# Optimization experiments

Hardware: AMD Instinct MI355X
Metric: run time of the kernel (lower is better)

The kernel has to match this reference:

```python
import jax, jax.numpy as jnp
import numpy as np

D_MODEL, H, G = 2048, 32, 8
D_K = D_MODEL // H          # 64
GROUP_SIZE = H // G         # 4
B, S = 2, 2048


def setup_inputs() -> dict:
    key = jax.random.key(0)
    ks = jax.random.split(key, 9)
    sd = 1.0 / np.sqrt(D_MODEL)
    x = jax.random.normal(ks[0], (B, S, D_MODEL), dtype=jnp.float32)
    Wq = jax.random.normal(ks[1], (D_MODEL, D_MODEL), dtype=jnp.float32) * sd
    bq = jax.random.normal(ks[2], (D_MODEL,), dtype=jnp.float32) * 0.01
    Wk = jax.random.normal(ks[3], (D_MODEL, G * D_K), dtype=jnp.float32) * sd
    bk = jax.random.normal(ks[4], (G * D_K,), dtype=jnp.float32) * 0.01
    Wv = jax.random.normal(ks[5], (D_MODEL, G * D_K), dtype=jnp.float32) * sd
    bv = jax.random.normal(ks[6], (G * D_K,), dtype=jnp.float32) * 0.01
    Wo = jax.random.normal(ks[7], (D_MODEL, D_MODEL), dtype=jnp.float32) * sd
    bo = jax.random.normal(ks[8], (D_MODEL,), dtype=jnp.float32) * 0.01
    return {"x": x, "Wq": Wq, "bq": bq, "Wk": Wk, "bk": bk,
            "Wv": Wv, "bv": bv, "Wo": Wo, "bo": bo}


def reference(x, Wq, bq, Wk, bk, Wv, bv, Wo, bo):
    Bsz, Sln, _ = x.shape
    # projections
    Q = (x @ Wq + bq).reshape(Bsz, Sln, H, D_K).transpose(0, 2, 1, 3)   # [B,h,S,dk]
    K = (x @ Wk + bk).reshape(Bsz, Sln, G, D_K).transpose(0, 2, 1, 3)   # [B,g,S,dk]
    V = (x @ Wv + bv).reshape(Bsz, Sln, G, D_K).transpose(0, 2, 1, 3)   # [B,g,S,dk]
    # reshape Q into groups: [B, g, group_size, S, dk]; K/V broadcast over group dim
    Qg = Q.reshape(Bsz, G, GROUP_SIZE, Sln, D_K)
    scores = jnp.einsum('bgmqd,bgkd->bgmqk', Qg, K) / jnp.sqrt(jnp.float32(D_K))
    attn = jax.nn.softmax(scores, axis=-1)                              # [B,g,gs,S,S]
    out = jnp.einsum('bgmqk,bgkd->bgmqd', attn, V)                      # [B,g,gs,S,dk]
    out = out.reshape(Bsz, H, Sln, D_K).transpose(0, 2, 1, 3).reshape(Bsz, Sln, D_MODEL)
    return out @ Wo + bo
```

## Files before the change

### kernel.cpp

```cpp
#include <hip/hip_runtime.h>
#include <stdint.h>

#define DMODEL 2048
#define NHEADS 32
#define NGRP 8
#define DKH 64
#define BATCH 2
#define SEQ 2048
#define MTOT (BATCH*SEQ)

typedef unsigned short u16;
typedef __bf16 bf16x8 __attribute__((ext_vector_type(8)));
typedef float f32x4 __attribute__((ext_vector_type(4)));
typedef _Float16 f16x4 __attribute__((ext_vector_type(4)));
typedef _Float16 f16x8 __attribute__((ext_vector_type(8)));

#define QSCALE 0.18033688011112042f

__device__ __forceinline__ u16 f2bf(float f){
    uint32_t x = __float_as_uint(f);
    x += 0x7FFFu + ((x >> 16) & 1u);
    return (u16)(x >> 16);
}

__device__ __forceinline__ void gld_lds16(const u16* g, u16* l){
    __builtin_amdgcn_global_load_lds(
        (const __attribute__((address_space(1))) uint32_t*)g,
        (__attribute__((address_space(3))) uint32_t*)l, 16, 0, 0);
}

__global__ void cvt_fused(const float* __restrict__ x, u16* __restrict__ xb,
                          const float* __restrict__ Wq, const float* __restrict__ Wk,
                          const float* __restrict__ Wv, const float* __restrict__ Wo,
                          u16* __restrict__ WqT, u16* __restrict__ WkT,
                          u16* __restrict__ WvT, u16* __restrict__ WoT){
    __shared__ float t[32][33];
    int bid = blockIdx.x;
    if (bid < 8192){
        int i = (bid * 256 + threadIdx.x) * 4;
        float4 v = *(const float4*)(x + i);
        uint32_t lo = (uint32_t)f2bf(v.x) | ((uint32_t)f2bf(v.y) << 16);
        uint32_t hi = (uint32_t)f2bf(v.z) | ((uint32_t)f2bf(v.w) << 16);
        *(uint2*)(xb + i) = make_uint2(lo, hi);
        return;
    }
    int id = bid - 8192;
    int bx = id % 160, ky = id / 160;
    const float* W; u16* T; int N; int cx;
    if (bx < 64)      { W = Wq; T = WqT; N = 2048; cx = bx; }
    else if (bx < 80) { W = Wk; T = WkT; N = 512;  cx = bx - 64; }
    else if (bx < 96) { W = Wv; T = WvT; N = 512;  cx = bx - 80; }
    else              { W = Wo; T = WoT; N = 2048; cx = bx - 96; }
    int tx = threadIdx.x & 31, ty = threadIdx.x >> 5;
    int n0 = cx * 32, k0 = ky * 32;
#pragma unroll
    for (int i = 0; i < 4; i++)
        t[ty*4+i][tx] = W[(size_t)(k0 + ty*4 + i) * N + n0 + tx];
    __syncthreads();
#pragma unroll
    for (int i = 0; i < 4; i++)
        T[(size_t)(n0 + ty*4 + i) * DMODEL + k0 + tx] = f2bf(t[tx][ty*4+i]);
}

template<int EPI, int MINW>
__global__ __launch_bounds__(256, MINW) void gemm_nt(
    const u16* __restrict__ A, const u16* __restrict__ Bt,
    const float* __restrict__ bias0, const float* __restrict__ bias1, const float* __restrict__ bias2,
    void* __restrict__ out0, void* __restrict__ out1, void* __restrict__ out2, int Kn)
{
    __shared__ alignas(16) u16 As[128*32];
    __shared__ alignas(16) u16 Bs[128*32];
    const int tid  = threadIdx.x;
    const int w    = tid >> 6, lane = tid & 63, quad = lane >> 4, l16 = lane & 15;
    const int wr   = w >> 1,  wc   = w & 1;

    int bid = blockIdx.y * gridDim.x + blockIdx.x;
    int nwg = gridDim.x * gridDim.y;
    int cpx = nwg >> 3;
    int sbid = (bid & 7) * cpx + (bid >> 3);
    int bx = sbid % gridDim.x, by = sbid / gridDim.x;
    const int m0 = bx * 128, n0 = by * 128;

    const int arow = lane >> 2, acol = (lane & 3) * 8;

    const u16* ga = A  + (size_t)(m0 + w*32 + arow) * Kn + acol;
    const u16* gb = Bt + (size_t)(n0 + w*32 + arow) * Kn + acol;
    u16* la = As + (w*32) * 32;
    u16* lb = Bs + (w*32) * 32;

    f32x4 acc[4][4] = {};

    for (int k0 = 0; k0 < Kn; k0 += 32){
        __syncthreads();
        gld_lds16(ga + k0,                  la);
        gld_lds16(ga + k0 + (size_t)16*Kn,  la + 16*32);
        gld_lds16(gb + k0,                  lb);
        gld_lds16(gb + k0 + (size_t)16*Kn,  lb + 16*32);
        __syncthreads();
        bf16x8 af[4], bfr[4];
#pragma unroll
        for (int t = 0; t < 4; t++)
            af[t]  = *(const bf16x8*)(As + (wr*64 + t*16 + l16)*32 + quad*8);
#pragma unroll
        for (int t = 0; t < 4; t++)
            bfr[t] = *(const bf16x8*)(Bs + (wc*64 + t*16 + l16)*32 + quad*8);
#pragma unroll
        for (int tm = 0; tm < 4; tm++)
#pragma unroll
            for (int tn = 0; tn < 4; tn++)
                acc[tm][tn] = __builtin_amdgcn_mfma_f32_16x16x32_bf16(af[tm], bfr[tn], acc[tm][tn], 0, 0, 0);
    }

#pragma unroll
    for (int tn = 0; tn < 4; tn++){
        int col = n0 + wc*64 + tn*16 + l16;
        float bv;
        if (EPI == 3) bv = (col < 2048) ? bias0[col] : (col < 2560) ? bias1[col-2048] : bias2[col-2560];
        else          bv = bias0[col];
#pragma unroll
        for (int tm = 0; tm < 4; tm++){
#pragma unroll
            for (int r = 0; r < 4; r++){
                int row = m0 + wr*64 + tm*16 + quad*4 + r;
                float v = acc[tm][tn][r] + bv;
                if (EPI == 3){
                    int b = row >> 11, s = row & (SEQ-1);
                    if (col < 2048){
                        int hh = col >> 6, d = col & 63;
                        ((u16*)out0)[(((size_t)b*NHEADS + hh)*SEQ + s)*DKH + d] = f2bf(v * QSCALE);
                    } else if (col < 2560){
                        int c = col - 2048, gg = c >> 6, d = c & 63;
                        ((u16*)out1)[(((size_t)b*NGRP + gg)*SEQ + s)*DKH + d] = f2bf(v);
                    } else {
                        int c = col - 2560, gg = c >> 6, d = c & 63;
                        int t = s & 31;
                        int pos = (t < 16) ? (((t >> 2) << 3) | (t & 3))
                                           : ((((t & 15) >> 2) << 3) | 4 | (t & 3));
                        int sp = (s & ~31) | pos;
                        ((u16*)out2)[(((size_t)b*NGRP + gg)*DKH + d)*SEQ + sp] =
                            __builtin_bit_cast(u16, (_Float16)v);
                    }
                } else {
                    ((float*)out0)[(size_t)row * DMODEL + col] = v;
                }
            }
        }
    }
}

__global__ __launch_bounds__(256, 4) void flash_kern(
    const u16* __restrict__ Qb, const u16* __restrict__ Kb,
    const u16* __restrict__ Vt, u16* __restrict__ Ob)
{
    __shared__ alignas(16) u16 Ks[2][64*64];
    __shared__ alignas(16) u16 Vs[2][64*64];
    const int tid = threadIdx.x, w = tid >> 6, lane = tid & 63;
    const int quad = lane >> 4, l16 = lane & 15;
    const int q0 = blockIdx.x * 128;
    const int h  = blockIdx.y, b = blockIdx.z, g = h >> 2;

    const u16* Qg = Qb + (((size_t)b*NHEADS + h)*SEQ + q0 + w*32) * DKH;
    const u16* Kg = Kb + ((size_t)b*NGRP + g) * SEQ * DKH;
    const u16* Vg = Vt + ((size_t)b*NGRP + g) * DKH * SEQ;

    const int lr = lane >> 3, lc = lane & 7;
    const int sw = lc ^ lr;
    const u16* gk0 = Kg + (size_t)(w*16 + lr) * DKH + sw*8;
    const u16* gv0 = Vg + (size_t)(w*16 + lr) * SEQ + sw*8;

    bf16x8 aq[2][2];
#pragma unroll
    for (int nt = 0; nt < 2; nt++)
#pragma unroll
        for (int ks = 0; ks < 2; ks++)
            aq[ks][nt] = *(const bf16x8*)(Qg + (nt*16 + l16)*DKH + ks*32 + quad*8);

    float lsum[2] = {};
    f32x4 oa[2][4] = {};

#define STAGE(buf, kt) do{                                                        \
        gld_lds16(gk0 + (size_t)(kt)*64*DKH,           Ks[buf] + (w*16)*64);      \
        gld_lds16(gk0 + (size_t)(kt)*64*DKH + 8*DKH,   Ks[buf] + (w*16+8)*64);    \
        gld_lds16(gv0 + (size_t)(kt)*64,               Vs[buf] + (w*16)*64);      \
        gld_lds16(gv0 + (size_t)(kt)*64 + (size_t)8*SEQ, Vs[buf] + (w*16+8)*64);  \
    }while(0)

#define COMPUTE(buf) do{                                                              \
        _Pragma("unroll")                                                             \
        for (int p = 0; p < 2; p++){                                                  \
            f16x4 pe[2], po[2];                                                       \
            _Pragma("unroll")                                                         \
            for (int hf = 0; hf < 2; hf++){                                           \
                const int kc = p*2 + hf;                                              \
                bf16x8 bk0 = *(const bf16x8*)(Ks[buf] + (kc*16 + l16)*64              \
                                              + ((quad     ^ (l16&7)) * 8));          \
                bf16x8 bk1 = *(const bf16x8*)(Ks[buf] + (kc*16 + l16)*64              \
                                              + (((4+quad) ^ (l16&7)) * 8));          \
                _Pragma("unroll")                                                     \
                for (int nt = 0; nt < 2; nt++){                                       \
                    f32x4 sa = {};                                                    \
                    sa = __builtin_amdgcn_mfma_f32_16x16x32_bf16(bk0, aq[0][nt], sa,0,0,0);\
                    sa = __builtin_amdgcn_mfma_f32_16x16x32_bf16(bk1, aq[1][nt], sa,0,0,0);\
                    float e0 = __builtin_amdgcn_exp2f(sa[0]);                         \
                    float e1 = __builtin_amdgcn_exp2f(sa[1]);                         \
                    float e2 = __builtin_amdgcn_exp2f(sa[2]);                         \
                    float e3 = __builtin_amdgcn_exp2f(sa[3]);                         \
                    lsum[nt] += (e0 + e1) + (e2 + e3);                                \
                    uint2 pk = make_uint2(                                            \
                        __builtin_bit_cast(uint32_t, __builtin_amdgcn_cvt_pkrtz(e0, e1)), \
                        __builtin_bit_cast(uint32_t, __builtin_amdgcn_cvt_pkrtz(e2, e3)));\
                    (hf ? po : pe)[nt] = __builtin_bit_cast(f16x4, pk);               \
                }                                                                     \
            }                                                                         \
            f16x8 pa8[2];                                                             \
            _Pragma("unroll")                                                         \
            for (int nt = 0; nt < 2; nt++)                                            \
                pa8[nt] = __builtin_shufflevector(pe[nt], po[nt], 0,1,2,3,4,5,6,7);   \
            _Pragma("unroll")                                                         \
            for (int dt = 0; dt < 4; dt++){                                           \
                f16x8 bv8 = *(const f16x8*)(Vs[buf] + (dt*16 + l16)*64                \
                             + (((4*p + quad) ^ (l16&7)) * 8));                       \
                _Pragma("unroll")                                                     \
                for (int nt = 0; nt < 2; nt++)                                        \
                    oa[nt][dt] = __builtin_amdgcn_mfma_f32_16x16x32_f16(              \
                        pa8[nt], bv8, oa[nt][dt], 0, 0, 0);                           \
            }                                                                         \
        }                                                                             \
    }while(0)

    STAGE(0, 0);
    __syncthreads();

    for (int kt2 = 0; kt2 < SEQ/128; ++kt2){
        int kt = kt2 * 2;
        STAGE(1, kt + 1);
        COMPUTE(0);
        __syncthreads();
        if (kt2 < SEQ/128 - 1) STAGE(0, kt + 2);
        COMPUTE(1);
        __syncthreads();
    }

#pragma unroll
    for (int nt = 0; nt < 2; nt++){
        float s = lsum[nt];
        s += __shfl_xor(s, 16, 64);
        s += __shfl_xor(s, 32, 64);
        lsum[nt] = 1.0f / s;
    }

#pragma unroll
    for (int nt = 0; nt < 2; nt++)
#pragma unroll
        for (int r = 0; r < 4; r++){
            float inv = __shfl(lsum[nt], quad*4 + r, 64);
            int q = q0 + w*32 + nt*16 + quad*4 + r;
#pragma unroll
            for (int dt = 0; dt < 4; dt++)
                Ob[((size_t)b*SEQ + q)*DMODEL + h*DKH + dt*16 + l16] = f2bf(oa[nt][dt][r] * inv);
        }
#undef STAGE
#undef COMPUTE
}


extern "C" void kernel_launch(void* const* d_in, const int* in_sizes, int n_in,
                              void* d_out, int out_size, void* d_ws, size_t ws_size,
                              hipStream_t stream)
{
    const float* x  = (const float*)d_in[0];
    const float* Wq = (const float*)d_in[1];
    const float* bq = (const float*)d_in[2];
    const float* Wk = (const float*)d_in[3];
    const float* bk = (const float*)d_in[4];
    const float* Wv = (const float*)d_in[5];
    const float* bv = (const float*)d_in[6];
    const float* Wo = (const float*)d_in[7];
    const float* bo = (const float*)d_in[8];

    uint8_t* p = (uint8_t*)d_ws;
    u16* xb  = (u16*)p; p += (size_t)MTOT*DMODEL*2;
    u16* WqT = (u16*)p; p += (size_t)DMODEL*DMODEL*2;
    u16* WkT = (u16*)p; p += (size_t)(NGRP*DKH)*DMODEL*2;
    u16* WvT = (u16*)p; p += (size_t)(NGRP*DKH)*DMODEL*2;
    u16* WoT = (u16*)p; p += (size_t)DMODEL*DMODEL*2;
    u16* Qb  = (u16*)p; p += (size_t)BATCH*NHEADS*SEQ*DKH*2;
    u16* Kb  = (u16*)p; p += (size_t)BATCH*NGRP*SEQ*DKH*2;
    u16* Vtb = (u16*)p; p += (size_t)BATCH*NGRP*DKH*SEQ*2;
    u16* Ob  = (u16*)p; p += (size_t)MTOT*DMODEL*2;

    cvt_fused<<<18432, 256, 0, stream>>>(x, xb, Wq, Wk, Wv, Wo, WqT, WkT, WvT, WoT);

    gemm_nt<3,3><<<dim3(MTOT/128, 3072/128), 256, 0, stream>>>(
        xb, WqT, bq, bk, bv, Qb, Kb, Vtb, DMODEL);

    flash_kern<<<dim3(SEQ/128, NHEADS, BATCH), 256, 0, stream>>>(Qb, Kb, Vtb, Ob);

    gemm_nt<2,2><<<dim3(MTOT/128, DMODEL/128), 256, 0, stream>>>(
        Ob, WoT, bo, nullptr, nullptr, d_out, nullptr, nullptr, DMODEL);
}
```

Baseline: 329.0 us.

## Double-buffer LDS tiles in GEMM to overlap global loads with MFMA

Turns the single-buffered shared-memory tiles of the bf16 GEMM into two ping-pong buffers. The next K-slice is issued with global-to-LDS loads while MFMAs run on the current slice, and one barrier per slice replaces two. The aim is to hide global memory latency behind compute. It doubles LDS use, which may lower occupancy, and it assumes Kn is a multiple of 64.

Result: slower. 337.9 us (+2.7%).

```diff
diff --git a/kernel.cpp b/kernel.cpp
--- a/kernel.cpp
+++ b/kernel.cpp
@@ -68,8 +68,8 @@
     const float* __restrict__ bias0, const float* __restrict__ bias1, const float* __restrict__ bias2,
     void* __restrict__ out0, void* __restrict__ out1, void* __restrict__ out2, int Kn)
 {
-    __shared__ alignas(16) u16 As[128*32];
-    __shared__ alignas(16) u16 Bs[128*32];
+    __shared__ alignas(16) u16 As[2][128*32];
+    __shared__ alignas(16) u16 Bs[2][128*32];
     const int tid  = threadIdx.x;
     const int w    = tid >> 6, lane = tid & 63, quad = lane >> 4, l16 = lane & 15;
     const int wr   = w >> 1,  wc   = w & 1;
@@ -85,31 +85,46 @@
 
     const u16* ga = A  + (size_t)(m0 + w*32 + arow) * Kn + acol;
     const u16* gb = Bt + (size_t)(n0 + w*32 + arow) * Kn + acol;
-    u16* la = As + (w*32) * 32;
-    u16* lb = Bs + (w*32) * 32;
 
     f32x4 acc[4][4] = {};
 
-    for (int k0 = 0; k0 < Kn; k0 += 32){
+#define GSTAGE(buf, k0) do{                                            \
+        gld_lds16(ga + (k0),                  As[buf] + (w*32)*32);    \
+        gld_lds16(ga + (k0) + (size_t)16*Kn,  As[buf] + (w*32+16)*32); \
+        gld_lds16(gb + (k0),                  Bs[buf] + (w*32)*32);    \
+        gld_lds16(gb + (k0) + (size_t)16*Kn,  Bs[buf] + (w*32+16)*32); \
+    }while(0)
+
+#define GCOMP(buf) do{                                                             \
+        bf16x8 af[4], bfr[4];                                                      \
+        _Pragma("unroll")                                                          \
+        for (int t = 0; t < 4; t++)                                                \
+            af[t]  = *(const bf16x8*)(As[buf] + (wr*64 + t*16 + l16)*32 + quad*8); \
+        _Pragma("unroll")                                                          \
+        for (int t = 0; t < 4; t++)                                                \
+            bfr[t] = *(const bf16x8*)(Bs[buf] + (wc*64 + t*16 + l16)*32 + quad*8); \
+        _Pragma("unroll")                                                          \
+        for (int tm = 0; tm < 4; tm++)                                             \
+            _Pragma("unroll")                                                      \
+            for (int tn = 0; tn < 4; tn++)                                         \
+                acc[tm][tn] = __builtin_amdgcn_mfma_f32_16x16x32_bf16(af[tm], bfr[tn], acc[tm][tn], 0, 0, 0); \
+    }while(0)
+
+    GSTAGE(0, 0);
+    __syncthreads();
+
+    for (int k2 = 0; k2 < Kn/64; k2++){
+        const int k0 = k2 * 64;
+        GSTAGE(1, k0 + 32);
+        GCOMP(0);
         __syncthreads();
-        gld_lds16(ga + k0,                  la);
-        gld_lds16(ga + k0 + (size_t)16*Kn,  la + 16*32);
-        gld_lds16(gb + k0,                  lb);
-        gld_lds16(gb + k0 + (size_t)16*Kn,  lb + 16*32);
+        if (k2 < Kn/64 - 1) GSTAGE(0, k0 + 64);
+        GCOMP(1);
         __syncthreads();
-        bf16x8 af[4], bfr[4];
-#pragma unroll
-        for (int t = 0; t < 4; t++)
-            af[t]  = *(const bf16x8*)(As + (wr*64 + t*16 + l16)*32 + quad*8);
-#pragma unroll
-        for (int t = 0; t < 4; t++)
-            bfr[t] = *(const bf16x8*)(Bs + (wc*64 + t*16 + l16)*32 + quad*8);
-#pragma unroll
-        for (int tm = 0; tm < 4; tm++)
-#pragma unroll
-            for (int tn = 0; tn < 4; tn++)
-                acc[tm][tn] = __builtin_amdgcn_mfma_f32_16x16x32_bf16(af[tm], bfr[tn], acc[tm][tn], 0, 0, 0);
-    }
+    }
+
+#undef GSTAGE
+#undef GCOMP
 
 #pragma unroll
     for (int tn = 0; tn < 4; tn++){
```
